# Kernel tuning notes

Hardware: AMD Instinct MI355X
Metric: run time of the kernel (lower is better)

The kernel has to match this reference:

```python
import jax, jax.numpy as jnp
import numpy as np


def setup_inputs() -> dict:
    key = jax.random.key(0)
    ks = jax.random.split(key, 6)
    B, C, H, W, Q = 16, 64, 64, 64, 8192
    HID = 256
    K = C * 9  # 576, unfolded channel count and srnet out_dim (co_mat=1)
    feat = jax.random.normal(ks[0], (B, C, H, W), jnp.float32)
    coord = jax.random.uniform(ks[1], (B, Q, 2), jnp.float32) * 2.0 - 1.0  # normalized [-1,1]
    cell = jnp.ones((B, Q, 2), jnp.float32) * (2.0 / 128.0)  # HR cell size for 128-px grid
    w1 = jax.random.normal(ks[2], (3, HID), jnp.float32) / np.sqrt(3.0)
    b1 = jnp.zeros((HID,), jnp.float32)
    w2 = jax.random.normal(ks[3], (HID, HID), jnp.float32) / np.sqrt(float(HID))
    b2 = jnp.zeros((HID,), jnp.float32)
    w3 = jax.random.normal(ks[4], (HID, K), jnp.float32) / np.sqrt(float(HID))
    b3 = jnp.zeros((K,), jnp.float32)
    return {"feat": feat, "coord": coord, "cell": cell,
            "w1": w1, "b1": b1, "w2": w2, "b2": b2, "w3": w3, "b3": b3}


def reference(feat, coord, cell, w1, b1, w2, b2, w3, b3):
    B, C, H, W = feat.shape
    Q = coord.shape[1]
    K = C * 9
    co_mat = 1
    # F.unfold(feat, 3, padding=1).view(B, C*9, H, W): channel-major, kernel pos minor
    padded = jnp.pad(feat, ((0, 0), (0, 0), (1, 1), (1, 1)))
    patches = jnp.stack([padded[:, :, i:i + H, j:j + W]
                         for i in range(3) for j in range(3)], axis=2)  # [B,C,9,H,W]
    featu = patches.reshape(B, K, H * W)
    # shift query coords by half a cell
    coord_ = coord - cell / 2.0
    coord_q = jnp.clip(coord_ + 1e-6, -1.0 + 1e-6, 1.0 - 1e-6)
    # nearest grid_sample, align_corners=False: idx = round(((c+1)*S - 1)/2)
    # coord[...,0] indexes H (grid y after flip), coord[...,1] indexes W (grid x)
    iy = jnp.clip(jnp.round(((coord_q[..., 0] + 1.0) * H - 1.0) / 2.0), 0, H - 1).astype(jnp.int32)
    ix = jnp.clip(jnp.round(((coord_q[..., 1] + 1.0) * W - 1.0) / 2.0), 0, W - 1).astype(jnp.int32)
    lin = iy * W + ix  # [B,Q]
    q_feat = jnp.take_along_axis(featu, lin[:, None, :], axis=2).transpose(0, 2, 1)  # [B,Q,K]
    # q_coord: make_coord value minus half-pixel shift at the nearest index = 2i/S - 1 (exact)
    qy = 2.0 * iy.astype(jnp.float32) / H - 1.0
    qx = 2.0 * ix.astype(jnp.float32) / W - 1.0
    rel_y = (coord_[..., 0] - qy) * (H / 2.0)
    rel_x = (coord_[..., 1] - qx) * (W / 2.0)
    r_rev = cell[..., 0] * (H / 2.0)
    inp = jnp.stack([rel_y, rel_x, r_rev], axis=-1)  # [B,Q,3]
    # srnet MLP: per-query filter of shape [K, co_mat]
    h = jax.nn.relu(inp @ w1 + b1)
    h = jax.nn.relu(h @ w2 + b2)
    wmat = (h @ w3 + b3).reshape(B, Q, K, co_mat)
    # bmm combine: [1,K] @ [K,co_mat] per query
    pred = jnp.einsum('bqk,bqkc->bqc', q_feat, wmat)  # [B,Q,1]
    return pred
```

## Files before the change

### kernel.cpp

```cpp
#include <hip/hip_runtime.h>
#include <hip/hip_bf16.h>

#define BB 16
#define CC 64
#define HH 64
#define WW 64
#define QQ 8192
#define HID 256
#define KK 576
#define HT 66
#define FROW 264

typedef short short8 __attribute__((ext_vector_type(8)));
typedef short sv4    __attribute__((ext_vector_type(4)));
typedef float f32x4  __attribute__((ext_vector_type(4)));

__device__ __forceinline__ short f2bf(float f) {
    union { float f; unsigned u; } v; v.f = f;
    unsigned r = v.u + 0x7fffu + ((v.u >> 16) & 1u);
    return (short)(r >> 16);
}
__device__ __forceinline__ float bf2f(short s) {
    union { unsigned u; float f; } v; v.u = ((unsigned)(unsigned short)s) << 16;
    return v.f;
}
__device__ __forceinline__ void glld16(const short* g, short* l) {
    __builtin_amdgcn_global_load_lds(
        (const __attribute__((address_space(1))) void*)g,
        (__attribute__((address_space(3))) void*)l, 16, 0, 0);
}

__global__ __launch_bounds__(256) void prep_transpose_k(const float* __restrict__ feat,
                                                        const float* __restrict__ w2,
                                                        const float* __restrict__ w3,
                                                        const float* __restrict__ b3,
                                                        short* __restrict__ featT,
                                                        short* __restrict__ w3cB,
                                                        short* __restrict__ w2cB) {
    __shared__ float ftile[64][65];
    const int t = threadIdx.x;
    const int gidx = blockIdx.x * 256 + t;

    if (gidx < 156672) {
        int kchunk = gidx / 2176;
        int rem = gidx - kchunk * 2176;
        int n = rem >> 3, j = rem & 7;
        int kglob = kchunk * 8 + j;
        int pos = kglob >> 6, c = kglob & 63;
        float v = 0.f;
        if (n < 256)      v = w3[n * KK + c * 9 + pos];
        else if (n == 256) v = b3[c * 9 + pos];
        w3cB[gidx] = f2bf(v);
    }
    if (gidx < 65536) {
        int kchunk = gidx >> 11;
        int rem = gidx & 2047;
        int n = rem >> 3, j = rem & 7;
        int k = kchunk * 8 + j;
        w2cB[gidx] = f2bf(w2[k * 256 + n]);
    }

    const int b = blockIdx.x / HT;
    const int yy = blockIdx.x - b * HT;
    short* out_row = featT + ((b * HT + yy) * HT) * 64;

    if (yy == 0 || yy == HT - 1) {
        for (int idx = t; idx < HT * 64; idx += 256) out_row[idx] = 0;
        return;
    }
    const int y = yy - 1;
    const float* src = feat + ((b * CC) * HH + y) * WW;
#pragma unroll
    for (int i = 0; i < 16; ++i) {
        int idx = i * 256 + t;
        int c = idx >> 6, x = idx & 63;
        ftile[c][x] = src[c * (HH * WW) + x];
    }
    if (t < 64) out_row[t] = 0;
    else if (t < 128) out_row[(HT - 1) * 64 + (t - 64)] = 0;
    __syncthreads();
#pragma unroll
    for (int i = 0; i < 16; ++i) {
        int idx = i * 256 + t;
        int x = idx >> 6, c = idx & 63;
        out_row[(x + 1) * 64 + c] = f2bf(ftile[c][x]);
    }
}

#define SSTR 72
__global__ __launch_bounds__(256, 2) void conv_k(const short* __restrict__ featT,
                                                 const short* __restrict__ w3cB,
                                                 short* __restrict__ F) {
    __shared__ short slab[3 * HT * SSTR];
    __shared__ short Bb[2][8704];
    const int t = threadIdx.x;
    const int wave = t >> 6, lane = t & 63, quad = lane >> 4, ln16 = lane & 15;
    const int b = blockIdx.x >> 6, y = blockIdx.x & 63;

    f32x4 acc[4][5];
#pragma unroll
    for (int a = 0; a < 4; ++a)
#pragma unroll
        for (int i = 0; i < 5; ++i) acc[a][i] = (f32x4){0.f, 0.f, 0.f, 0.f};

    auto stageB = [&](int buf, int st) {
        const short* src = w3cB + st * 8704;
#pragma unroll
        for (int u = 0; u < 5; ++u) {
            int cidx = (u < 4) ? (u * 4 + wave) : 16;
            if (u < 4 || wave == 0)
                glld16(src + cidx * 512 + lane * 8, &Bb[buf][cidx * 512]);
        }
    };

    stageB(0, 0);

    const short* slabsrc = featT + b * (HT * HT * 64) + y * (HT * 64);
#pragma unroll
    for (int it = 0; it < 7; ++it) {
        int i = it * 256 + t;
        if (i < 1584) {
            short8 v = *(const short8*)(slabsrc + i * 8);
            int row = i >> 3, cs = (i & 7) * 8;
            *(short8*)(&slab[row * SSTR + cs]) = v;
        }
    }
    __syncthreads();

#pragma unroll
    for (int st = 0; st < 18; ++st) {
        const int cur = st & 1;
        if (st < 17) stageB(cur ^ 1, st + 1);
        const int pos = st >> 1, ks = st & 1;
        const int di = pos / 3, dj = pos - di * 3;
        short8 af[4];
#pragma unroll
        for (int ms = 0; ms < 4; ++ms)
            af[ms] = *(const short8*)(&slab[(di * HT + ms * 16 + ln16 + dj) * SSTR + ks * 32 + quad * 8]);
#pragma unroll
        for (int i = 0; i < 5; ++i) {
            int sub = (i < 4) ? (wave + 4 * i) : 16;
            short8 bf = *(const short8*)(&Bb[cur][(quad * 272 + sub * 16 + ln16) * 8]);
#pragma unroll
            for (int ms = 0; ms < 4; ++ms)
                acc[ms][i] = __builtin_amdgcn_mfma_f32_16x16x32_bf16(af[ms], bf, acc[ms][i], 0, 0, 0);
        }
        __syncthreads();
    }

#pragma unroll
    for (int h = 0; h < 2; ++h) {
#pragma unroll
        for (int i = 0; i < 5; ++i) {
            int sub = (i < 4) ? (wave + 4 * i) : 16;
            int n = sub * 16 + ln16;
            bool store = (i < 4) || (wave == 0 && n < FROW);
            if (store) {
#pragma unroll
                for (int ms2 = 0; ms2 < 2; ++ms2) {
                    int ms = h * 2 + ms2;
#pragma unroll
                    for (int r = 0; r < 4; ++r) {
                        int xl = ms2 * 16 + quad * 4 + r;
                        slab[xl * FROW + n] = f2bf(acc[ms][i][r]);
                    }
                }
            }
        }
        __syncthreads();
        short8* dst = (short8*)(F + ((long)(b * 64 + y) * 64 + h * 32) * FROW);
        const short8* src8 = (const short8*)slab;
#pragma unroll
        for (int it = 0; it < 5; ++it) {
            int idx = it * 256 + t;
            if (idx < (32 * FROW) / 8) dst[idx] = src8[idx];
        }
        __syncthreads();
    }
}

#define HSTRIDE 264
__global__ __launch_bounds__(256, 2) void mlp_k(const float* __restrict__ coord,
                                                const float* __restrict__ cell,
                                                const float* __restrict__ w1,
                                                const float* __restrict__ b1,
                                                const float* __restrict__ b2v,
                                                const short* __restrict__ w2cB,
                                                const short* __restrict__ F,
                                                float* __restrict__ out) {
    __shared__ short H_lds[64 * HSTRIDE];
    __shared__ short Wb[2][8192];
    __shared__ float red_s[64][4];

    const int t = threadIdx.x;
    const int wave = t >> 6, lane = t & 63, quad = lane >> 4, ln16 = lane & 15;
    const int qbase = blockIdx.x * 64;
    const int b = qbase >> 13;

    auto stageW = [&](int buf, int s) {
        const short* src = w2cB + s * 8192;
#pragma unroll
        for (int u = 0; u < 4; ++u) {
            int cidx = u * 4 + wave;
            glld16(src + cidx * 512 + lane * 8, &Wb[buf][cidx * 512]);
        }
    };

    stageW(0, 0);

    const int g = qbase + lane;
    const float2 cc = *(const float2*)(coord + g * 2);
    const float2 ce = *(const float2*)(cell + g * 2);
    const float coy = cc.x - ce.x * 0.5f, cox = cc.y - ce.y * 0.5f;
    const float cqy = fminf(fmaxf(coy + 1e-6f, -0.999999f), 0.999999f);
    const float cqx = fminf(fmaxf(cox + 1e-6f, -0.999999f), 0.999999f);
    int iy = (int)rintf(((cqy + 1.0f) * 64.0f - 1.0f) * 0.5f); iy = min(max(iy, 0), 63);
    int ix = (int)rintf(((cqx + 1.0f) * 64.0f - 1.0f) * 0.5f); ix = min(max(ix, 0), 63);
    const int lin = iy * 64 + ix;
    const float in0 = (coy - ((float)iy * (1.0f / 32.0f) - 1.0f)) * 32.0f;
    const float in1 = (cox - ((float)ix * (1.0f / 32.0f) - 1.0f)) * 32.0f;
    const float in2 = ce.x * 32.0f;

    const int k0w = wave * 64;
#pragma unroll
    for (int c8 = 0; c8 < 8; ++c8) {
        const int k0 = k0w + c8 * 8;
        f32x4 wa0 = *(const f32x4*)(w1 + k0),       wa1 = *(const f32x4*)(w1 + k0 + 4);
        f32x4 wb0 = *(const f32x4*)(w1 + 256 + k0), wb1 = *(const f32x4*)(w1 + 256 + k0 + 4);
        f32x4 wc0 = *(const f32x4*)(w1 + 512 + k0), wc1 = *(const f32x4*)(w1 + 512 + k0 + 4);
        f32x4 bb0 = *(const f32x4*)(b1 + k0),       bb1 = *(const f32x4*)(b1 + k0 + 4);
        short8 hv;
#pragma unroll
        for (int jj = 0; jj < 4; ++jj) {
            float v0 = fmaf(in0, wa0[jj], fmaf(in1, wb0[jj], fmaf(in2, wc0[jj], bb0[jj])));
            float v1 = fmaf(in0, wa1[jj], fmaf(in1, wb1[jj], fmaf(in2, wc1[jj], bb1[jj])));
            hv[jj]     = f2bf(fmaxf(v0, 0.f));
            hv[jj + 4] = f2bf(fmaxf(v1, 0.f));
        }
        *(short8*)(&H_lds[lane * HSTRIDE + k0]) = hv;
    }
    f32x4 b2q[4];
#pragma unroll
    for (int i = 0; i < 4; ++i)
        b2q[i] = *(const f32x4*)(b2v + wave * 64 + i * 16 + quad * 4);
    __syncthreads();

    f32x4 acc2[4][4];
#pragma unroll
    for (int i = 0; i < 4; ++i)
#pragma unroll
        for (int ms = 0; ms < 4; ++ms) acc2[i][ms] = (f32x4){0.f, 0.f, 0.f, 0.f};
#pragma unroll
    for (int s = 0; s < 8; ++s) {
        const int cur = s & 1;
        if (s < 7) stageW(cur ^ 1, s + 1);
        short8 wf[4], hf[4];
#pragma unroll
        for (int i = 0; i < 4; ++i)
            wf[i] = *(const short8*)(&Wb[cur][(quad * 256 + wave * 64 + i * 16 + ln16) * 8]);
#pragma unroll
        for (int ms = 0; ms < 4; ++ms)
            hf[ms] = *(const short8*)(&H_lds[(ms * 16 + ln16) * HSTRIDE + s * 32 + quad * 8]);
#pragma unroll
        for (int i = 0; i < 4; ++i)
#pragma unroll
            for (int ms = 0; ms < 4; ++ms)
                acc2[i][ms] = __builtin_amdgcn_mfma_f32_16x16x32_bf16(wf[i], hf[ms], acc2[i][ms], 0, 0, 0);
        __syncthreads();
    }

    const short* Fb = F + (long)b * 4096 * FROW;
    sv4 fv[4][4];
#pragma unroll
    for (int ms = 0; ms < 4; ++ms) {
        int linm = __shfl(lin, ms * 16 + ln16, 64);
        const short* Fr = Fb + (long)linm * FROW + wave * 64 + quad * 4;
#pragma unroll
        for (int i = 0; i < 4; ++i) fv[ms][i] = *(const sv4*)(Fr + i * 16);
    }
    const float fbv = bf2f(Fb[(long)lin * FROW + 256]);

    float part[4] = {0.f, 0.f, 0.f, 0.f};
#pragma unroll
    for (int i = 0; i < 4; ++i)
#pragma unroll
        for (int ms = 0; ms < 4; ++ms)
#pragma unroll
            for (int r = 0; r < 4; ++r)
                part[ms] = fmaf(fmaxf(acc2[i][ms][r] + b2q[i][r], 0.f), bf2f(fv[ms][i][r]), part[ms]);
#pragma unroll
    for (int ms = 0; ms < 4; ++ms) {
        part[ms] += __shfl_xor(part[ms], 16, 64);
        part[ms] += __shfl_xor(part[ms], 32, 64);
    }
    if (quad == 0) {
#pragma unroll
        for (int ms = 0; ms < 4; ++ms) red_s[ms * 16 + ln16][wave] = part[ms];
    }
    __syncthreads();
    if (t < 64)
        out[qbase + t] = red_s[t][0] + red_s[t][1] + red_s[t][2] + red_s[t][3] + fbv;
}

extern "C" void kernel_launch(void* const* d_in, const int* in_sizes, int n_in,
                              void* d_out, int out_size, void* d_ws, size_t ws_size,
                              hipStream_t stream) {
    const float* feat  = (const float*)d_in[0];
    const float* coord = (const float*)d_in[1];
    const float* cell  = (const float*)d_in[2];
    const float* w1    = (const float*)d_in[3];
    const float* b1    = (const float*)d_in[4];
    const float* w2    = (const float*)d_in[5];
    const float* b2    = (const float*)d_in[6];
    const float* w3    = (const float*)d_in[7];
    const float* b3    = (const float*)d_in[8];
    float* out = (float*)d_out;

    char* ws = (char*)d_ws;
    short* w3cB  = (short*)(ws);
    short* w2cB  = (short*)(ws + 313344);
    short* featT = (short*)(ws + 444416);
    short* F     = (short*)(ws + 9365504);
    (void)ws_size; (void)in_sizes; (void)n_in; (void)out_size;

    prep_transpose_k<<<BB * HT, 256, 0, stream>>>(feat, w2, w3, b3, featT, w3cB, w2cB);
    conv_k<<<BB * HH, 256, 0, stream>>>(featT, w3cB, F);
    mlp_k<<<(BB * QQ) / 64, 256, 0, stream>>>(coord, cell, w1, b1, b2, w2cB, F, out);
}
```

Before: 158.3 us.

## Halve H LDS buffer by staging hidden activations in two phases

The layer-1 activation tile held in LDS is halved: waves 0-1 write their half of the hidden activations first, and waves 2-3 keep theirs in registers and write them after the first four K-steps of the layer-2 MFMA loop. This lowers LDS per block, which may allow more resident blocks per CU. It also drops the trailing barrier of the last loop iteration and uses a lighter LDS-only barrier. In exchange it costs 32 extra VGPRs per thread for the held activations and adds a mid-loop serialization point.

New measurement: 157.7 us. Within noise of the previous version (-0.4%).

```diff
diff --git a/kernel.cpp b/kernel.cpp
--- a/kernel.cpp
+++ b/kernel.cpp
@@ -23,6 +23,11 @@
 __device__ __forceinline__ float bf2f(short s) {
     union { unsigned u; float f; } v; v.u = ((unsigned)(unsigned short)s) << 16;
     return v.f;
+}
+__device__ __forceinline__ void barrier_lds() {
+    asm volatile("s_waitcnt lgkmcnt(0)" ::: "memory");
+    __builtin_amdgcn_s_barrier();
+    asm volatile("" ::: "memory");
 }
 __device__ __forceinline__ void glld16(const short* g, short* l) {
     __builtin_amdgcn_global_load_lds(
@@ -179,7 +184,7 @@
     }
 }
 
-#define HSTRIDE 264
+#define HSPLIT 136
 __global__ __launch_bounds__(256, 2) void mlp_k(const float* __restrict__ coord,
                                                 const float* __restrict__ cell,
                                                 const float* __restrict__ w1,
@@ -188,7 +193,7 @@
                                                 const short* __restrict__ w2cB,
                                                 const short* __restrict__ F,
                                                 float* __restrict__ out) {
-    __shared__ short H_lds[64 * HSTRIDE];
+    __shared__ short Hh[64 * HSPLIT];
     __shared__ short Wb[2][8192];
     __shared__ float red_s[64][4];
 
@@ -221,6 +226,7 @@
     const float in1 = (cox - ((float)ix * (1.0f / 32.0f) - 1.0f)) * 32.0f;
     const float in2 = ce.x * 32.0f;
 
+    short8 hv[8];
     const int k0w = wave * 64;
 #pragma unroll
     for (int c8 = 0; c8 < 8; ++c8) {
@@ -229,15 +235,18 @@
         f32x4 wb0 = *(const f32x4*)(w1 + 256 + k0), wb1 = *(const f32x4*)(w1 + 256 + k0 + 4);
         f32x4 wc0 = *(const f32x4*)(w1 + 512 + k0), wc1 = *(const f32x4*)(w1 + 512 + k0 + 4);
         f32x4 bb0 = *(const f32x4*)(b1 + k0),       bb1 = *(const f32x4*)(b1 + k0 + 4);
-        short8 hv;
 #pragma unroll
         for (int jj = 0; jj < 4; ++jj) {
             float v0 = fmaf(in0, wa0[jj], fmaf(in1, wb0[jj], fmaf(in2, wc0[jj], bb0[jj])));
             float v1 = fmaf(in0, wa1[jj], fmaf(in1, wb1[jj], fmaf(in2, wc1[jj], bb1[jj])));
-            hv[jj]     = f2bf(fmaxf(v0, 0.f));
-            hv[jj + 4] = f2bf(fmaxf(v1, 0.f));
-        }
-        *(short8*)(&H_lds[lane * HSTRIDE + k0]) = hv;
+            hv[c8][jj]     = f2bf(fmaxf(v0, 0.f));
+            hv[c8][jj + 4] = f2bf(fmaxf(v1, 0.f));
+        }
+    }
+    if (wave < 2) {
+#pragma unroll
+        for (int c8 = 0; c8 < 8; ++c8)
+            *(short8*)(&Hh[lane * HSPLIT + wave * 64 + c8 * 8]) = hv[c8];
     }
     f32x4 b2q[4];
 #pragma unroll
@@ -258,15 +267,26 @@
 #pragma unroll
         for (int i = 0; i < 4; ++i)
             wf[i] = *(const short8*)(&Wb[cur][(quad * 256 + wave * 64 + i * 16 + ln16) * 8]);
+        const int col = (s & 3) * 32 + quad * 8;
 #pragma unroll
         for (int ms = 0; ms < 4; ++ms)
-            hf[ms] = *(const short8*)(&H_lds[(ms * 16 + ln16) * HSTRIDE + s * 32 + quad * 8]);
+            hf[ms] = *(const short8*)(&Hh[(ms * 16 + ln16) * HSPLIT + col]);
 #pragma unroll
         for (int i = 0; i < 4; ++i)
 #pragma unroll
             for (int ms = 0; ms < 4; ++ms)
                 acc2[i][ms] = __builtin_amdgcn_mfma_f32_16x16x32_bf16(wf[i], hf[ms], acc2[i][ms], 0, 0, 0);
-        __syncthreads();
+        if (s == 3) {
+            __syncthreads();
+            if (wave >= 2) {
+#pragma unroll
+                for (int c8 = 0; c8 < 8; ++c8)
+                    *(short8*)(&Hh[lane * HSPLIT + (wave - 2) * 64 + c8 * 8]) = hv[c8];
+            }
+            barrier_lds();
+        } else if (s < 7) {
+            __syncthreads();
+        }
     }
 
     const short* Fb = F + (long)b * 4096 * FROW;
@@ -297,7 +317,7 @@
 #pragma unroll
         for (int ms = 0; ms < 4; ++ms) red_s[ms * 16 + ln16][wave] = part[ms];
     }
-    __syncthreads();
+    barrier_lds();
     if (t < 64)
         out[qbase + t] = red_s[t][0] + red_s[t][1] + red_s[t][2] + red_s[t][3] + fbv;
 }
```
